# Kernel tuning notes

Measured on AMD Instinct MI355X. Metric: run time of the kernel, lower is better.

The kernel has to match this reference:

```python
import jax, jax.numpy as jnp
import numpy as np

DIM = 1024
HEADS = 16
DH = DIM // HEADS          # 64
SEQ_LEN = 4096
LATENT = 1024
HIST = SEQ_LEN - LATENT    # 3072
LN_EPS = 1e-5


def setup_inputs() -> dict:
    key = jax.random.key(0)
    ks = jax.random.split(key, 5)
    b = 2
    x = jax.random.normal(ks[0], (b, SEQ_LEN, DIM), dtype=jnp.float32)
    s = 0.02
    Wq = jax.random.normal(ks[1], (DIM, DIM), dtype=jnp.float32) * s
    Wkv = jax.random.normal(ks[2], (DIM, DIM), dtype=jnp.float32) * s
    Wo = jax.random.normal(ks[3], (DIM, DIM), dtype=jnp.float32) * s
    bo = jnp.zeros((DIM,), dtype=jnp.float32)
    gamma = jnp.ones((DH,), dtype=jnp.float32)
    beta = jnp.zeros((DH,), dtype=jnp.float32)
    return {"x": x, "Wq": Wq, "Wkv": Wkv, "Wo": Wo, "bo": bo,
            "gamma": gamma, "beta": beta}


def _rotate_half(t):
    t1, t2 = jnp.split(t, 2, axis=-1)
    return jnp.concatenate([-t2, t1], axis=-1)


def reference(x, Wq, Wkv, Wo, bo, gamma, beta):
    b, n, dim = x.shape
    # projections (nn.Linear: y = x @ W.T), split heads -> (b, h, n, d)
    q = jnp.einsum('bnd,ed->bne', x, Wq).reshape(b, n, HEADS, DH).transpose(0, 2, 1, 3)
    kv = jnp.einsum('bnd,ed->bne', x, Wkv).reshape(b, n, HEADS, DH).transpose(0, 2, 1, 3)

    # layer_num == 0: queries only for the latent segment
    q = q[:, :, HIST:, :]  # (b, h, latent, d)

    # rotary embeddings: concat-style freqs over head dim
    inv_freq = 1.0 / (10000.0 ** (jnp.arange(0, DH, 2, dtype=jnp.float32) / DH))
    freqs = jnp.arange(n, dtype=jnp.float32)[:, None] * inv_freq[None, :]  # (n, DH/2)
    emb = jnp.concatenate([freqs, freqs], axis=-1)  # (n, DH)
    cos, sin = jnp.cos(emb), jnp.sin(emb)
    q = q * cos[HIST:] + _rotate_half(q) * sin[HIST:]
    kv = kv * cos + _rotate_half(kv) * sin

    q = q * (DH ** -0.5)

    # per-kv LayerNorm over head dim
    mu = kv.mean(axis=-1, keepdims=True)
    var = ((kv - mu) ** 2).mean(axis=-1, keepdims=True)
    kvn = (kv - mu) * jax.lax.rsqrt(var + LN_EPS) * gamma + beta

    attn = jnp.einsum('bhid,bhjd->bhij', q, kvn)  # (b, h, latent, n)

    # causal mask only on latent columns: col j (>= HIST) masked if j-HIST > i
    i = jnp.arange(LATENT)[:, None]
    j = jnp.arange(n)[None, :]
    mask = (j - HIST) > i  # false for history columns (j < HIST)
    neg = -jnp.finfo(attn.dtype).max
    attn = jnp.where(mask, neg, attn)

    attn = jax.nn.softmax(attn, axis=-1)
    out = jnp.einsum('bhij,bhjd->bhid', attn, kvn)  # (b, h, latent, d)
    out = out.transpose(0, 2, 1, 3).reshape(b, LATENT, dim)
    return jnp.einsum('bnd,ed->bne', out, Wo) + bo
```

## Files before the change

kernel.cpp:

```cpp
#include <hip/hip_runtime.h>
#include <hip/hip_bf16.h>
#include <cstdint>

#define DIMC 1024
#define HEADS 16
#define DHH 64
#define SEQ 4096
#define LATENT 1024
#define HISTC 3072
#define BATCH 2

typedef __attribute__((ext_vector_type(8))) __bf16 bf16x8;
typedef __attribute__((ext_vector_type(4))) float f32x4;
typedef __attribute__((ext_vector_type(16))) float f32x16;

__global__ void k_prep(const float* __restrict__ x, const float* __restrict__ Wq,
                       const float* __restrict__ Wkv, const float* __restrict__ Wo,
                       __bf16* __restrict__ x16, __bf16* __restrict__ wq16,
                       __bf16* __restrict__ wkv16, __bf16* __restrict__ wo16,
                       float2* __restrict__ cs) {
  int bidx = blockIdx.x;
  if (bidx < 2048) {
    int base = bidx * 256 + threadIdx.x;
#pragma unroll
    for (int k = 0; k < 4; ++k) {
      int i = base + k * 524288;
      float4 v = reinterpret_cast<const float4*>(x)[i];
      union { __bf16 h[4]; uint64_t u; } p;
      p.h[0] = (__bf16)v.x; p.h[1] = (__bf16)v.y;
      p.h[2] = (__bf16)v.z; p.h[3] = (__bf16)v.w;
      reinterpret_cast<uint64_t*>(x16)[i] = p.u;
    }
  } else if (bidx < 3584) {
    int id = bidx - 2048;
    const float* src; __bf16* dst;
    if (id < 512) { src = Wq; dst = wq16; }
    else if (id < 1024) { src = Wkv; dst = wkv16; id -= 512; }
    else { src = Wo; dst = wo16; id -= 1024; }
#pragma unroll
    for (int k = 0; k < 2; ++k) {
      int idx = id * 512 + k * 256 + threadIdx.x;
      float4 v = reinterpret_cast<const float4*>(src)[idx];
      union { __bf16 h[4]; uint64_t u; } p;
      p.h[0] = (__bf16)v.x; p.h[1] = (__bf16)v.y;
      p.h[2] = (__bf16)v.z; p.h[3] = (__bf16)v.w;
      reinterpret_cast<uint64_t*>(dst)[idx] = p.u;
    }
  } else {
    int idx = (bidx - 3584) * 256 + threadIdx.x;
    int pos = idx >> 5, f = idx & 31;
    float invf = exp2f(-(float)f * 0.41524101186f);
    float s, c;
    sincosf((float)pos * invf, &s, &c);
    cs[idx] = make_float2(c, s);
  }
}

__device__ __forceinline__ void gload16(void* lds, const void* g) {
  __builtin_amdgcn_global_load_lds(
      (const __attribute__((address_space(1))) unsigned int*)g,
      (__attribute__((address_space(3))) unsigned int*)lds, 16, 0, 0);
}

template<int BIAS>
__launch_bounds__(256)
__global__ void k_gemm(const __bf16* __restrict__ A, const __bf16* __restrict__ Bw,
                       float* __restrict__ C, const float* __restrict__ bias,
                       int M, int N, int K) {
  __shared__ __align__(16) char lds[16384];
  const int t = threadIdx.x;
  const int l = t & 63, w = t >> 6;
  const int wr = w >> 1, wc = w & 1;
  const int mblocks = M >> 7;
  const int m0 = (blockIdx.x % mblocks) * 128, n0 = (blockIdx.x / mblocks) * 128;
  const int lrow = l & 15, lk = l >> 4;
  f32x4 acc[4][4] = {};

  for (int k0 = 0; k0 < K; k0 += 32) {
    if (k0) __syncthreads();
#pragma unroll
    for (int i = 0; i < 2; ++i) {
      int c = i * 256 + t;
      int row = c >> 2, kc = c & 3;
      gload16(lds + c * 16, A + (size_t)(m0 + row) * K + k0 + kc * 8);
      gload16(lds + 8192 + c * 16, Bw + (size_t)(n0 + row) * K + k0 + kc * 8);
    }
    __syncthreads();
    bf16x8 af[4], bfr[4];
#pragma unroll
    for (int m = 0; m < 4; ++m)
      af[m] = *reinterpret_cast<const bf16x8*>(lds + (wr * 64 + m * 16 + lrow) * 64 + lk * 16);
#pragma unroll
    for (int n = 0; n < 4; ++n)
      bfr[n] = *reinterpret_cast<const bf16x8*>(lds + 8192 + (wc * 64 + n * 16 + lrow) * 64 + lk * 16);
#pragma unroll
    for (int m = 0; m < 4; ++m)
#pragma unroll
      for (int n = 0; n < 4; ++n)
        acc[m][n] = __builtin_amdgcn_mfma_f32_16x16x32_bf16(af[m], bfr[n], acc[m][n], 0, 0, 0);
  }

#pragma unroll
  for (int m = 0; m < 4; ++m)
#pragma unroll
    for (int n = 0; n < 4; ++n)
#pragma unroll
      for (int r = 0; r < 4; ++r) {
        int row = m0 + wr * 64 + m * 16 + (l >> 4) * 4 + r;
        int col = n0 + wc * 64 + n * 16 + (l & 15);
        float v = acc[m][n][r];
        if (BIAS) v += bias[col];
        C[(size_t)row * N + col] = v;
      }
}

__launch_bounds__(256)
__global__ void k_gemmqkv(const __bf16* __restrict__ x16,
                          const __bf16* __restrict__ wkv16,
                          const __bf16* __restrict__ wq16,
                          __bf16* __restrict__ kvn, __bf16* __restrict__ kvnT,
                          __bf16* __restrict__ qb,
                          const float* __restrict__ gamma,
                          const float* __restrict__ beta,
                          const float2* __restrict__ cstab) {
  __shared__ __align__(16) char lds[16384];
  const int t = threadIdx.x, l = t & 63, w = t >> 6;
  const int wr = w >> 1, wc = w & 1;
  const int by = blockIdx.x % 80;
  const bool isq = by >= 64;
  const int m0 = (isq ? (by - 64) : by) * 128;
  const int n0 = (blockIdx.x / 80) * 128;
  const __bf16* Bw = isq ? wq16 : wkv16;
  const int lrow = l & 15, lk = l >> 4;
  f32x4 acc[4][4] = {};

  for (int k0 = 0; k0 < 1024; k0 += 32) {
    if (k0) __syncthreads();
#pragma unroll
    for (int i = 0; i < 2; ++i) {
      int c = i * 256 + t;
      int row = c >> 2, kc = c & 3;
      int mi = m0 + row;
      if (isq) mi += HISTC + (mi >> 10) * HISTC;
      gload16(lds + c * 16, x16 + (size_t)mi * 1024 + k0 + kc * 8);
      gload16(lds + 8192 + c * 16, Bw + (size_t)(n0 + row) * 1024 + k0 + kc * 8);
    }
    __syncthreads();
    bf16x8 af[4], bfr[4];
#pragma unroll
    for (int m = 0; m < 4; ++m)
      af[m] = *reinterpret_cast<const bf16x8*>(lds + (wr * 64 + m * 16 + lrow) * 64 + lk * 16);
#pragma unroll
    for (int n = 0; n < 4; ++n)
      bfr[n] = *reinterpret_cast<const bf16x8*>(lds + 8192 + (wc * 64 + n * 16 + lrow) * 64 + lk * 16);
#pragma unroll
    for (int m = 0; m < 4; ++m)
#pragma unroll
      for (int n = 0; n < 4; ++n)
        acc[m][n] = __builtin_amdgcn_mfma_f32_16x16x32_bf16(af[m], bfr[n], acc[m][n], 0, 0, 0);
  }

#pragma unroll
  for (int m = 0; m < 4; ++m)
#pragma unroll
    for (int r = 0; r < 4; ++r) {
      int rl = wr * 64 + m * 16 + lk * 4 + r;
      int pos = isq ? (HISTC + ((m0 + rl) & 1023)) : ((m0 + rl) & 4095);
      float2 cs0 = cstab[pos * 32 + lrow];
      float2 cs1 = cstab[pos * 32 + 16 + lrow];
      float a0 = acc[m][0][r], a2 = acc[m][2][r];
      acc[m][0][r] = a0 * cs0.x - a2 * cs0.y;
      acc[m][2][r] = a2 * cs0.x + a0 * cs0.y;
      float a1 = acc[m][1][r], a3 = acc[m][3][r];
      acc[m][1][r] = a1 * cs1.x - a3 * cs1.y;
      acc[m][3][r] = a3 * cs1.x + a1 * cs1.y;
    }

  const int h = (n0 + wc * 64) >> 6;
  if (!isq) {
    float g4[4], b4[4];
#pragma unroll
    for (int n = 0; n < 4; ++n) { g4[n] = gamma[n * 16 + lrow]; b4[n] = beta[n * 16 + lrow]; }
#pragma unroll
    for (int m = 0; m < 4; ++m)
#pragma unroll
      for (int r = 0; r < 4; ++r) {
        float s1 = acc[m][0][r] + acc[m][1][r] + acc[m][2][r] + acc[m][3][r];
        float s2 = acc[m][0][r] * acc[m][0][r] + acc[m][1][r] * acc[m][1][r] +
                   acc[m][2][r] * acc[m][2][r] + acc[m][3][r] * acc[m][3][r];
#pragma unroll
        for (int mk = 1; mk < 16; mk <<= 1) {
          s1 += __shfl_xor(s1, mk);
          s2 += __shfl_xor(s2, mk);
        }
        float mu = s1 * 0.015625f;
        float var = s2 * 0.015625f - mu * mu;
        float inv = rsqrtf(var + 1e-5f);
#pragma unroll
        for (int n = 0; n < 4; ++n)
          acc[m][n][r] = (acc[m][n][r] - mu) * inv * g4[n] + b4[n];
      }
    const size_t hb = (size_t)((m0 >> 12) * HEADS + h);
#pragma unroll
    for (int m = 0; m < 4; ++m)
#pragma unroll
      for (int r = 0; r < 4; ++r) {
        int pos = (m0 + wr * 64 + m * 16 + lk * 4 + r) & 4095;
#pragma unroll
        for (int n = 0; n < 4; ++n)
          kvn[(hb * SEQ + pos) * DHH + n * 16 + lrow] = (__bf16)acc[m][n][r];
      }
#pragma unroll
    for (int m = 0; m < 4; ++m) {
      int pos0 = (m0 + wr * 64 + m * 16 + lk * 4) & 4095;
      int sp = (pos0 & ~12) | ((pos0 & 4) << 1) | ((pos0 & 8) >> 1);
#pragma unroll
      for (int n = 0; n < 4; ++n) {
        union { __bf16 hh[4]; uint64_t u; } pk;
#pragma unroll
        for (int r = 0; r < 4; ++r) pk.hh[r] = (__bf16)acc[m][n][r];
        *reinterpret_cast<uint64_t*>(kvnT + (hb * DHH + n * 16 + lrow) * SEQ + sp) = pk.u;
      }
    }
  } else {
    const size_t hb = (size_t)((m0 >> 10) * HEADS + h);
#pragma unroll
    for (int m = 0; m < 4; ++m)
#pragma unroll
      for (int r = 0; r < 4; ++r) {
        int qi = (m0 + wr * 64 + m * 16 + lk * 4 + r) & 1023;
#pragma unroll
        for (int n = 0; n < 4; ++n)
          qb[(hb * LATENT + qi) * DHH + n * 16 + lrow] =
              (__bf16)(acc[m][n][r] * 0.18033688011112042f);
      }
  }
}

__device__ __forceinline__ float fexp2(float x) {
#if __has_builtin(__builtin_amdgcn_exp2f)
  return __builtin_amdgcn_exp2f(x);
#else
  return exp2f(x);
#endif
}

__device__ __forceinline__ unsigned pk2(float a, float b) {
  union { __bf16 h[2]; unsigned u; } x;
  x.h[0] = (__bf16)a; x.h[1] = (__bf16)b;
  return x.u;
}

template<int NJ>
__launch_bounds__(256)
__global__ void k_flash12(const __bf16* __restrict__ qb, const __bf16* __restrict__ kvn,
                          const __bf16* __restrict__ kvnT, float* __restrict__ part) {
  const int bid = blockIdx.x;
  const int xcd = bid & 7;
  const int u = bid >> 3;
  const int jq = u % NJ;
  const int rest = u / NJ;
  int itq = rest & 7;
  const int grpb = rest >> 3;
  if (grpb >= 2) itq = 7 - itq;
  const int bh = xcd + 8 * grpb;
  const int h = bh & 15, b = bh >> 4;
  const int t = threadIdx.x, l = t & 63, w = t >> 6;
  const int q = l & 31, hi = l >> 5;
  const int iw0 = itq * 128;
  const int iwv = iw0 + w * 32;
  const int i = iwv + q;
  const __bf16* qbase = qb + ((size_t)(b * HEADS + h) * LATENT + iwv) * DHH;
  const __bf16* kbase = kvn + (size_t)(b * HEADS + h) * SEQ * DHH;
  const __bf16* vbase = kvnT + (size_t)(b * HEADS + h) * DHH * SEQ;

  __shared__ __align__(16) __bf16 Kl[2][2][32][64];
  __shared__ __align__(16) __bf16 Vl[2][2][64][32];

  const int krow = t >> 3, kgc = ((t & 7) ^ (krow & 7)) * 8;
  const int vrow = t >> 2, vgc = ((t & 3) ^ (vrow & 3)) * 8;

  bf16x8 qf[4];
#pragma unroll
  for (int c = 0; c < 4; ++c)
    qf[c] = *reinterpret_cast<const bf16x8*>(qbase + (size_t)q * DHH + c * 16 + hi * 8);

  const f32x16 Z = {};
  f32x16 O0 = {}, O1 = {};
  float m_run = -INFINITY, lacc = 0.f;

  const int ng = 2 * itq + 50;
  const int g0 = (ng * jq) / NJ, g1 = (ng * (jq + 1)) / NJ;
  const int sx = q & 3;

  {
    const int ja = g0 * 64;
    gload16((char*)&Kl[0][0][0][0] + t * 16, kbase + (size_t)(ja + krow) * DHH + kgc);
    gload16((char*)&Kl[0][1][0][0] + t * 16, kbase + (size_t)(ja + 32 + krow) * DHH + kgc);
    gload16((char*)&Vl[0][0][0][0] + t * 16, vbase + (size_t)vrow * SEQ + ja + vgc);
    gload16((char*)&Vl[0][1][0][0] + t * 16, vbase + (size_t)vrow * SEQ + ja + 32 + vgc);
  }
  __syncthreads();

  for (int g = g0; g < g1; ++g) {
    const int cur = (g - g0) & 1;
    const int ja = g * 64, jb = ja + 32;
    const char* Ka = (const char*)&Kl[cur][0][0][0];
    const char* Va = (const char*)&Vl[cur][0][0][0];
    bf16x8 kf0 = *reinterpret_cast<const bf16x8*>(Ka + q * 128 + ((0 + hi) ^ (q & 7)) * 16);
    bf16x8 kf1 = *reinterpret_cast<const bf16x8*>(Ka + q * 128 + ((2 + hi) ^ (q & 7)) * 16);
    bf16x8 kf2 = *reinterpret_cast<const bf16x8*>(Ka + q * 128 + ((4 + hi) ^ (q & 7)) * 16);
    bf16x8 kf3 = *reinterpret_cast<const bf16x8*>(Ka + q * 128 + ((6 + hi) ^ (q & 7)) * 16);
    f32x16 S = __builtin_amdgcn_mfma_f32_32x32x16_bf16(kf0, qf[0], Z, 0, 0, 0);
    S = __builtin_amdgcn_mfma_f32_32x32x16_bf16(kf1, qf[1], S, 0, 0, 0);
    S = __builtin_amdgcn_mfma_f32_32x32x16_bf16(kf2, qf[2], S, 0, 0, 0);
    S = __builtin_amdgcn_mfma_f32_32x32x16_bf16(kf3, qf[3], S, 0, 0, 0);
    if (g + 1 < g1) {
      const int jn = (g + 1) * 64;
      gload16((char*)&Kl[cur ^ 1][0][0][0] + t * 16, kbase + (size_t)(jn + krow) * DHH + kgc);
      gload16((char*)&Kl[cur ^ 1][1][0][0] + t * 16, kbase + (size_t)(jn + 32 + krow) * DHH + kgc);
      gload16((char*)&Vl[cur ^ 1][0][0][0] + t * 16, vbase + (size_t)vrow * SEQ + jn + vgc);
      gload16((char*)&Vl[cur ^ 1][1][0][0] + t * 16, vbase + (size_t)vrow * SEQ + jn + 32 + vgc);
    }
    if (ja + 31 > iwv + HISTC) {
#pragma unroll
      for (int r = 0; r < 16; ++r) {
        int j = ja + (r & 3) + 8 * (r >> 2) + 4 * hi;
        if (j > i + HISTC) S[r] = -1e30f;
      }
    }
    {
      float u1 = fmaxf(fmaxf(S[0], S[1]), S[2]);
      float u2 = fmaxf(fmaxf(S[3], S[4]), S[5]);
      float u3 = fmaxf(fmaxf(S[6], S[7]), S[8]);
      float u4 = fmaxf(fmaxf(S[9], S[10]), S[11]);
      float u5 = fmaxf(fmaxf(S[12], S[13]), S[14]);
      float pm = fmaxf(fmaxf(fmaxf(u1, u2), u3), fmaxf(fmaxf(u4, u5), S[15]));
      if (__any(pm > m_run + 8.0f)) {
        pm = fmaxf(pm, __shfl_xor(pm, 32));
        float mn = fmaxf(m_run, pm);
        float sc = fexp2(m_run - mn);
        m_run = mn;
        lacc *= sc;
#pragma unroll
        for (int r = 0; r < 16; ++r) { O0[r] *= sc; O1[r] *= sc; }
      }
      float p[16];
#pragma unroll
      for (int r = 0; r < 16; ++r) p[r] = fexp2(S[r] - m_run);
      float s8[8];
#pragma unroll
      for (int r = 0; r < 8; ++r) s8[r] = p[r] + p[r + 8];
      lacc += ((s8[0] + s8[4]) + (s8[1] + s8[5])) + ((s8[2] + s8[6]) + (s8[3] + s8[7]));
      union { unsigned u[4]; bf16x8 v; } pf0, pf1;
      pf0.u[0] = pk2(p[0], p[1]);   pf0.u[1] = pk2(p[2], p[3]);
      pf0.u[2] = pk2(p[4], p[5]);   pf0.u[3] = pk2(p[6], p[7]);
      pf1.u[0] = pk2(p[8], p[9]);   pf1.u[1] = pk2(p[10], p[11]);
      pf1.u[2] = pk2(p[12], p[13]); pf1.u[3] = pk2(p[14], p[15]);
      bf16x8 va00 = *reinterpret_cast<const bf16x8*>(Va + q * 64 + (hi ^ sx) * 16);
      bf16x8 va01 = *reinterpret_cast<const bf16x8*>(Va + q * 64 + ((2 + hi) ^ sx) * 16);
      bf16x8 va10 = *reinterpret_cast<const bf16x8*>(Va + (32 + q) * 64 + (hi ^ sx) * 16);
      bf16x8 va11 = *reinterpret_cast<const bf16x8*>(Va + (32 + q) * 64 + ((2 + hi) ^ sx) * 16);
      O0 = __builtin_amdgcn_mfma_f32_32x32x16_bf16(va00, pf0.v, O0, 0, 0, 0);
      O0 = __builtin_amdgcn_mfma_f32_32x32x16_bf16(va01, pf1.v, O0, 0, 0, 0);
      O1 = __builtin_amdgcn_mfma_f32_32x32x16_bf16(va10, pf0.v, O1, 0, 0, 0);
      O1 = __builtin_amdgcn_mfma_f32_32x32x16_bf16(va11, pf1.v, O1, 0, 0, 0);
    }
    const char* Kb = (const char*)&Kl[cur][1][0][0];
    const char* Vb = (const char*)&Vl[cur][1][0][0];
    bf16x8 kg0 = *reinterpret_cast<const bf16x8*>(Kb + q * 128 + ((0 + hi) ^ (q & 7)) * 16);
    bf16x8 kg1 = *reinterpret_cast<const bf16x8*>(Kb + q * 128 + ((2 + hi) ^ (q & 7)) * 16);
    bf16x8 kg2 = *reinterpret_cast<const bf16x8*>(Kb + q * 128 + ((4 + hi) ^ (q & 7)) * 16);
    bf16x8 kg3 = *reinterpret_cast<const bf16x8*>(Kb + q * 128 + ((6 + hi) ^ (q & 7)) * 16);
    f32x16 T = __builtin_amdgcn_mfma_f32_32x32x16_bf16(kg0, qf[0], Z, 0, 0, 0);
    T = __builtin_amdgcn_mfma_f32_32x32x16_bf16(kg1, qf[1], T, 0, 0, 0);
    T = __builtin_amdgcn_mfma_f32_32x32x16_bf16(kg2, qf[2], T, 0, 0, 0);
    T = __builtin_amdgcn_mfma_f32_32x32x16_bf16(kg3, qf[3], T, 0, 0, 0);
    if (jb + 31 > iwv + HISTC) {
#pragma unroll
      for (int r = 0; r < 16; ++r) {
        int j = jb + (r & 3) + 8 * (r >> 2) + 4 * hi;
        if (j > i + HISTC) T[r] = -1e30f;
      }
    }
    {
      float u1 = fmaxf(fmaxf(T[0], T[1]), T[2]);
      float u2 = fmaxf(fmaxf(T[3], T[4]), T[5]);
      float u3 = fmaxf(fmaxf(T[6], T[7]), T[8]);
      float u4 = fmaxf(fmaxf(T[9], T[10]), T[11]);
      float u5 = fmaxf(fmaxf(T[12], T[13]), T[14]);
      float pm = fmaxf(fmaxf(fmaxf(u1, u2), u3), fmaxf(fmaxf(u4, u5), T[15]));
      if (__any(pm > m_run + 8.0f)) {
        pm = fmaxf(pm, __shfl_xor(pm, 32));
        float mn = fmaxf(m_run, pm);
        float sc = fexp2(m_run - mn);
        m_run = mn;
        lacc *= sc;
#pragma unroll
        for (int r = 0; r < 16; ++r) { O0[r] *= sc; O1[r] *= sc; }
      }
      float p[16];
#pragma unroll
      for (int r = 0; r < 16; ++r) p[r] = fexp2(T[r] - m_run);
      float s8[8];
#pragma unroll
      for (int r = 0; r < 8; ++r) s8[r] = p[r] + p[r + 8];
      lacc += ((s8[0] + s8[4]) + (s8[1] + s8[5])) + ((s8[2] + s8[6]) + (s8[3] + s8[7]));
      union { unsigned u[4]; bf16x8 v; } pf0, pf1;
      pf0.u[0] = pk2(p[0], p[1]);   pf0.u[1] = pk2(p[2], p[3]);
      pf0.u[2] = pk2(p[4], p[5]);   pf0.u[3] = pk2(p[6], p[7]);
      pf1.u[0] = pk2(p[8], p[9]);   pf1.u[1] = pk2(p[10], p[11]);
      pf1.u[2] = pk2(p[12], p[13]); pf1.u[3] = pk2(p[14], p[15]);
      bf16x8 vb00 = *reinterpret_cast<const bf16x8*>(Vb + q * 64 + (hi ^ sx) * 16);
      bf16x8 vb01 = *reinterpret_cast<const bf16x8*>(Vb + q * 64 + ((2 + hi) ^ sx) * 16);
      bf16x8 vb10 = *reinterpret_cast<const bf16x8*>(Vb + (32 + q) * 64 + (hi ^ sx) * 16);
      bf16x8 vb11 = *reinterpret_cast<const bf16x8*>(Vb + (32 + q) * 64 + ((2 + hi) ^ sx) * 16);
      O0 = __builtin_amdgcn_mfma_f32_32x32x16_bf16(vb00, pf0.v, O0, 0, 0, 0);
      O0 = __builtin_amdgcn_mfma_f32_32x32x16_bf16(vb01, pf1.v, O0, 0, 0, 0);
      O1 = __builtin_amdgcn_mfma_f32_32x32x16_bf16(vb10, pf0.v, O1, 0, 0, 0);
      O1 = __builtin_amdgcn_mfma_f32_32x32x16_bf16(vb11, pf1.v, O1, 0, 0, 0);
    }
    __syncthreads();
  }
  float l_run = lacc + __shfl_xor(lacc, 32);

  const int pidx = (bh * 8 + itq) * NJ + jq;
  float* pw = part + (size_t)(pidx * 4 + w) * 34 * 64;
#pragma unroll
  for (int r = 0; r < 16; ++r) pw[r * 64 + l] = O0[r];
#pragma unroll
  for (int r = 0; r < 16; ++r) pw[(16 + r) * 64 + l] = O1[r];
  pw[32 * 64 + l] = m_run;
  pw[33 * 64 + l] = l_run;
}

template<int NJ>
__global__ void k_fmerge12(const float* __restrict__ part, __bf16* __restrict__ aout) {
  const int u = blockIdx.x;
  const int bh = u >> 3, itq = u & 7;
  const int b = bh >> 4, h = bh & 15;
  const int t = threadIdx.x;
  const int w = t >> 6, sub = t & 63, q = sub & 31, hi = sub >> 5;
  const float* pp[NJ];
#pragma unroll
  for (int j = 0; j < NJ; ++j)
    pp[j] = part + (size_t)((u * NJ + j) * 4 + w) * 34 * 64;
  float mm = -INFINITY;
#pragma unroll
  for (int j = 0; j < NJ; ++j) mm = fmaxf(mm, pp[j][32 * 64 + sub]);
  float sc[NJ];
  float ll = 0.f;
#pragma unroll
  for (int j = 0; j < NJ; ++j) {
    sc[j] = fexp2(pp[j][32 * 64 + sub] - mm);
    ll += pp[j][33 * 64 + sub] * sc[j];
  }
  float inv = 1.f / ll;
  const int row = itq * 128 + w * 32 + q;
  __bf16* orow = aout + ((size_t)(b * LATENT) + row) * DIMC + h * DHH;
#pragma unroll
  for (int g = 0; g < 4; ++g) {
    union { __bf16 hh[4]; uint2 u2; } pk;
#pragma unroll
    for (int e = 0; e < 4; ++e) {
      float o = 0.f;
#pragma unroll
      for (int j = 0; j < NJ; ++j) o += pp[j][(4 * g + e) * 64 + sub] * sc[j];
      pk.hh[e] = (__bf16)(o * inv);
    }
    *reinterpret_cast<uint2*>(orow + 8 * g + 4 * hi) = pk.u2;
#pragma unroll
    for (int e = 0; e < 4; ++e) {
      float o = 0.f;
#pragma unroll
      for (int j = 0; j < NJ; ++j) o += pp[j][(16 + 4 * g + e) * 64 + sub] * sc[j];
      pk.hh[e] = (__bf16)(o * inv);
    }
    *reinterpret_cast<uint2*>(orow + 32 + 8 * g + 4 * hi) = pk.u2;
  }
}

extern "C" void kernel_launch(void* const* d_in, const int* in_sizes, int n_in,
                              void* d_out, int out_size, void* d_ws, size_t ws_size,
                              hipStream_t stream) {
  const float* x = (const float*)d_in[0];
  const float* Wq = (const float*)d_in[1];
  const float* Wkv = (const float*)d_in[2];
  const float* Wo = (const float*)d_in[3];
  const float* bo = (const float*)d_in[4];
  const float* gamma = (const float*)d_in[5];
  const float* beta = (const float*)d_in[6];

  char* ws = (char*)d_ws;
  size_t o = 0;
  __bf16* x16 = (__bf16*)(ws + o);  o += (size_t)BATCH * SEQ * DIMC * 2;
  __bf16* wq16 = (__bf16*)(ws + o); o += (size_t)DIMC * DIMC * 2;
  __bf16* wkv16 = (__bf16*)(ws + o); o += (size_t)DIMC * DIMC * 2;
  __bf16* wo16 = (__bf16*)(ws + o); o += (size_t)DIMC * DIMC * 2;
  float2* cstab = (float2*)(ws + o); o += (size_t)SEQ * 32 * 8;
  __bf16* kvn = (__bf16*)(ws + o);  o += (size_t)BATCH * HEADS * SEQ * DHH * 2;
  __bf16* kvnT = (__bf16*)(ws + o); o += (size_t)BATCH * HEADS * SEQ * DHH * 2;
  __bf16* qb = (__bf16*)(ws + o);   o += (size_t)BATCH * HEADS * LATENT * DHH * 2;
  __bf16* aout = (__bf16*)(ws + o); o += (size_t)BATCH * LATENT * DIMC * 2;
  float* part = (float*)(ws + o);
  const size_t part4 = (size_t)1024 * 4 * 34 * 64 * 4;
  const bool use4 = (ws_size - o) >= part4;

  k_prep<<<4096, 256, 0, stream>>>(x, Wq, Wkv, Wo, x16, wq16, wkv16, wo16, cstab);
  k_gemmqkv<<<640, 256, 0, stream>>>(x16, wkv16, wq16, kvn, kvnT, qb, gamma, beta, cstab);
  if (use4) {
    k_flash12<4><<<1024, 256, 0, stream>>>(qb, kvn, kvnT, part);
    k_fmerge12<4><<<256, 256, 0, stream>>>(part, aout);
  } else {
    k_flash12<2><<<512, 256, 0, stream>>>(qb, kvn, kvnT, part);
    k_fmerge12<2><<<256, 256, 0, stream>>>(part, aout);
  }
  k_gemm<1><<<128, 256, 0, stream>>>(aout, wo16, (float*)d_out, bo, 2048, 1024, 1024);
}
```

Before: 152.9 us.

## Double GEMM K-tile to 64 with XOR-swizzled LDS and fix flash split to 2

Both GEMM kernels now stage a 64-wide K slice per iteration instead of 32, which halves the number of barrier and load rounds. They also apply an XOR swizzle to the LDS layout so the wider rows avoid bank conflicts on fragment reads. The attention path drops the runtime choice between a 4-way and a 2-way KV split and always uses the 2-way split. This trades some parallelism in the flash kernel for less merge work and a fixed workspace size. The larger LDS footprint per block may reduce how many blocks fit on each compute unit.

New measurement: 141.3 us (median of 2 runs). 7.5% less time.

```diff
diff --git a/kernel.cpp b/kernel.cpp
--- a/kernel.cpp
+++ b/kernel.cpp
@@ -67,7 +67,7 @@
 __global__ void k_gemm(const __bf16* __restrict__ A, const __bf16* __restrict__ Bw,
                        float* __restrict__ C, const float* __restrict__ bias,
                        int M, int N, int K) {
-  __shared__ __align__(16) char lds[16384];
+  __shared__ __align__(16) char lds[32768];
   const int t = threadIdx.x;
   const int l = t & 63, w = t >> 6;
   const int wr = w >> 1, wc = w & 1;
@@ -76,28 +76,38 @@
   const int lrow = l & 15, lk = l >> 4;
   f32x4 acc[4][4] = {};
 
-  for (int k0 = 0; k0 < K; k0 += 32) {
+  for (int k0 = 0; k0 < K; k0 += 64) {
     if (k0) __syncthreads();
 #pragma unroll
-    for (int i = 0; i < 2; ++i) {
+    for (int i = 0; i < 4; ++i) {
       int c = i * 256 + t;
-      int row = c >> 2, kc = c & 3;
-      gload16(lds + c * 16, A + (size_t)(m0 + row) * K + k0 + kc * 8);
-      gload16(lds + 8192 + c * 16, Bw + (size_t)(n0 + row) * K + k0 + kc * 8);
+      int row = c >> 3;
+      int kgc = ((c & 7) ^ (row & 7)) * 8;
+      gload16(lds + c * 16, A + (size_t)(m0 + row) * K + k0 + kgc);
+      gload16(lds + 16384 + c * 16, Bw + (size_t)(n0 + row) * K + k0 + kgc);
     }
     __syncthreads();
-    bf16x8 af[4], bfr[4];
-#pragma unroll
-    for (int m = 0; m < 4; ++m)
-      af[m] = *reinterpret_cast<const bf16x8*>(lds + (wr * 64 + m * 16 + lrow) * 64 + lk * 16);
-#pragma unroll
-    for (int n = 0; n < 4; ++n)
-      bfr[n] = *reinterpret_cast<const bf16x8*>(lds + 8192 + (wc * 64 + n * 16 + lrow) * 64 + lk * 16);
-#pragma unroll
-    for (int m = 0; m < 4; ++m)
-#pragma unroll
-      for (int n = 0; n < 4; ++n)
-        acc[m][n] = __builtin_amdgcn_mfma_f32_16x16x32_bf16(af[m], bfr[n], acc[m][n], 0, 0, 0);
+#pragma unroll
+    for (int ks = 0; ks < 2; ++ks) {
+      bf16x8 af[4], bfr[4];
+#pragma unroll
+      for (int m = 0; m < 4; ++m) {
+        int row = wr * 64 + m * 16 + lrow;
+        af[m] = *reinterpret_cast<const bf16x8*>(
+            lds + row * 128 + ((ks * 4 + lk) ^ (row & 7)) * 16);
+      }
+#pragma unroll
+      for (int n = 0; n < 4; ++n) {
+        int row = wc * 64 + n * 16 + lrow;
+        bfr[n] = *reinterpret_cast<const bf16x8*>(
+            lds + 16384 + row * 128 + ((ks * 4 + lk) ^ (row & 7)) * 16);
+      }
+#pragma unroll
+      for (int m = 0; m < 4; ++m)
+#pragma unroll
+        for (int n = 0; n < 4; ++n)
+          acc[m][n] = __builtin_amdgcn_mfma_f32_16x16x32_bf16(af[m], bfr[n], acc[m][n], 0, 0, 0);
+    }
   }
 
 #pragma unroll
@@ -123,7 +133,7 @@
                           const float* __restrict__ gamma,
                           const float* __restrict__ beta,
                           const float2* __restrict__ cstab) {
-  __shared__ __align__(16) char lds[16384];
+  __shared__ __align__(16) char lds[32768];
   const int t = threadIdx.x, l = t & 63, w = t >> 6;
   const int wr = w >> 1, wc = w & 1;
   const int by = blockIdx.x % 80;
@@ -134,30 +144,40 @@
   const int lrow = l & 15, lk = l >> 4;
   f32x4 acc[4][4] = {};
 
-  for (int k0 = 0; k0 < 1024; k0 += 32) {
+  for (int k0 = 0; k0 < 1024; k0 += 64) {
     if (k0) __syncthreads();
 #pragma unroll
-    for (int i = 0; i < 2; ++i) {
+    for (int i = 0; i < 4; ++i) {
       int c = i * 256 + t;
-      int row = c >> 2, kc = c & 3;
+      int row = c >> 3;
+      int kgc = ((c & 7) ^ (row & 7)) * 8;
       int mi = m0 + row;
       if (isq) mi += HISTC + (mi >> 10) * HISTC;
-      gload16(lds + c * 16, x16 + (size_t)mi * 1024 + k0 + kc * 8);
-      gload16(lds + 8192 + c * 16, Bw + (size_t)(n0 + row) * 1024 + k0 + kc * 8);
+      gload16(lds + c * 16, x16 + (size_t)mi * 1024 + k0 + kgc);
+      gload16(lds + 16384 + c * 16, Bw + (size_t)(n0 + row) * 1024 + k0 + kgc);
     }
     __syncthreads();
-    bf16x8 af[4], bfr[4];
-#pragma unroll
-    for (int m = 0; m < 4; ++m)
-      af[m] = *reinterpret_cast<const bf16x8*>(lds + (wr * 64 + m * 16 + lrow) * 64 + lk * 16);
-#pragma unroll
-    for (int n = 0; n < 4; ++n)
-      bfr[n] = *reinterpret_cast<const bf16x8*>(lds + 8192 + (wc * 64 + n * 16 + lrow) * 64 + lk * 16);
-#pragma unroll
-    for (int m = 0; m < 4; ++m)
-#pragma unroll
-      for (int n = 0; n < 4; ++n)
-        acc[m][n] = __builtin_amdgcn_mfma_f32_16x16x32_bf16(af[m], bfr[n], acc[m][n], 0, 0, 0);
+#pragma unroll
+    for (int ks = 0; ks < 2; ++ks) {
+      bf16x8 af[4], bfr[4];
+#pragma unroll
+      for (int m = 0; m < 4; ++m) {
+        int row = wr * 64 + m * 16 + lrow;
+        af[m] = *reinterpret_cast<const bf16x8*>(
+            lds + row * 128 + ((ks * 4 + lk) ^ (row & 7)) * 16);
+      }
+#pragma unroll
+      for (int n = 0; n < 4; ++n) {
+        int row = wc * 64 + n * 16 + lrow;
+        bfr[n] = *reinterpret_cast<const bf16x8*>(
+            lds + 16384 + row * 128 + ((ks * 4 + lk) ^ (row & 7)) * 16);
+      }
+#pragma unroll
+      for (int m = 0; m < 4; ++m)
+#pragma unroll
+        for (int n = 0; n < 4; ++n)
+          acc[m][n] = __builtin_amdgcn_mfma_f32_16x16x32_bf16(af[m], bfr[n], acc[m][n], 0, 0, 0);
+    }
   }
 
 #pragma unroll
@@ -502,18 +522,11 @@
   __bf16* kvnT = (__bf16*)(ws + o); o += (size_t)BATCH * HEADS * SEQ * DHH * 2;
   __bf16* qb = (__bf16*)(ws + o);   o += (size_t)BATCH * HEADS * LATENT * DHH * 2;
   __bf16* aout = (__bf16*)(ws + o); o += (size_t)BATCH * LATENT * DIMC * 2;
-  float* part = (float*)(ws + o);
-  const size_t part4 = (size_t)1024 * 4 * 34 * 64 * 4;
-  const bool use4 = (ws_size - o) >= part4;
+  float* part = (float*)(ws + o);   o += (size_t)512 * 4 * 34 * 64 * 4;
 
   k_prep<<<4096, 256, 0, stream>>>(x, Wq, Wkv, Wo, x16, wq16, wkv16, wo16, cstab);
   k_gemmqkv<<<640, 256, 0, stream>>>(x16, wkv16, wq16, kvn, kvnT, qb, gamma, beta, cstab);
-  if (use4) {
-    k_flash12<4><<<1024, 256, 0, stream>>>(qb, kvn, kvnT, part);
-    k_fmerge12<4><<<256, 256, 0, stream>>>(part, aout);
-  } else {
-    k_flash12<2><<<512, 256, 0, stream>>>(qb, kvn, kvnT, part);
-    k_fmerge12<2><<<256, 256, 0, stream>>>(part, aout);
-  }
+  k_flash12<2><<<512, 256, 0, stream>>>(qb, kvn, kvnT, part);
+  k_fmerge12<2><<<256, 256, 0, stream>>>(part, aout);
   k_gemm<1><<<128, 256, 0, stream>>>(aout, wo16, (float*)d_out, bo, 2048, 1024, 1024);
 }
```
